# Optimization experiments

Measured on AMD Instinct MI355X. Metric: run time of the kernel, lower is better.

## Reference

```python
import jax, jax.numpy as jnp
import numpy as np

N_PROP, N_GRID, N_KEY, C_FEAT = 128, 216, 4096, 128
RADII = (0.8, 1.6)
NSAMPLES = (16, 16)
C_OUT = 64  # per-branch MLP output channels


def setup_inputs() -> dict:
    key = jax.random.key(0)
    ks = jax.random.split(key, 20)
    s = 0.05
    return {
        "wlh": jax.random.uniform(ks[0], (N_PROP, 3)) * 4.0 + 0.5,
        "center": jax.random.normal(ks[1], (N_PROP, 3)) * 5.0,
        "yaw": jax.random.uniform(ks[2], (N_PROP,)) * 2.0 * np.pi,
        "u": jax.random.uniform(ks[3], (N_PROP, N_GRID, 3)),
        "keypoints_xyz": jax.random.normal(ks[4], (1, N_KEY, 3)) * 5.0,
        "keypoints_features": jax.random.normal(ks[5], (1, C_FEAT, N_KEY)),
        "pn0_w1": jax.random.normal(ks[6], (C_OUT, C_FEAT + 3)) * s,
        "pn0_g1": jnp.ones((C_OUT,)), "pn0_b1": jnp.zeros((C_OUT,)),
        "pn0_w2": jax.random.normal(ks[7], (C_OUT, C_OUT)) * s,
        "pn0_g2": jnp.ones((C_OUT,)), "pn0_b2": jnp.zeros((C_OUT,)),
        "pn1_w1": jax.random.normal(ks[8], (C_OUT, C_FEAT + 3)) * s,
        "pn1_g1": jnp.ones((C_OUT,)), "pn1_b1": jnp.zeros((C_OUT,)),
        "pn1_w2": jax.random.normal(ks[9], (C_OUT, C_OUT)) * s,
        "pn1_g2": jnp.ones((C_OUT,)), "pn1_b2": jnp.zeros((C_OUT,)),
        "red_w1": jax.random.normal(ks[10], (256, N_GRID * 2 * C_OUT)) * 0.01,
        "red_b1": jnp.zeros((256,)),
        "red_w2": jax.random.normal(ks[11], (256, 256)) * s,
        "red_b2": jnp.zeros((256,)),
    }


def reference(wlh, center, yaw, u, keypoints_xyz, keypoints_features,
              pn0_w1, pn0_g1, pn0_b1, pn0_w2, pn0_g2, pn0_b2,
              pn1_w1, pn1_g1, pn1_b1, pn1_w2, pn1_g2, pn1_b2,
              red_w1, red_b1, red_w2, red_b2):
    n, m, _ = u.shape
    # --- sample gridpoints inside proposals and rotate by yaw around z ---
    gp = u * wlh[:, None, :]                                 # (n, m, 3)
    c, s = jnp.cos(yaw), jnp.sin(yaw)
    R = jnp.stack([c, -s, s, c], axis=-1).reshape(-1, 2, 2)   # (n, 2, 2)
    xy = jnp.einsum('njk,nmk->nmj', R, gp[..., :2])
    grid = jnp.concatenate([xy, gp[..., 2:]], -1) + center[:, None, :]
    grid = grid.reshape(-1, 3)                               # (G, 3), G = n*m

    kp = keypoints_xyz[0]                                    # (K, 3)
    kf = jnp.transpose(keypoints_features[0])                # (K, C)
    K = kp.shape[0]

    # squared distances (G, K) without materializing (G, K, 3)
    d2 = (jnp.sum(grid * grid, -1)[:, None]
          + jnp.sum(kp * kp, -1)[None, :]
          - 2.0 * grid @ kp.T)

    def ball_query(radius, nsample):
        # first `nsample` in-radius indices in original order; pad with first
        # hit; all-zeros if no point in radius (pointnet2 CUDA semantics).
        mask = d2 < radius * radius
        cand = jnp.where(mask, jnp.arange(K, dtype=jnp.int32), K)
        srt = jnp.sort(cand, axis=-1)[:, :nsample]           # (G, ns)
        first = srt[:, :1]
        return jnp.where(srt < K, srt, jnp.where(first < K, first, 0))

    def branch(radius, nsample, w1, g1, b1, w2, g2, b2):
        idx = ball_query(radius, nsample)                    # (G, ns)
        xyz = kp[idx] - grid[:, None, :]                     # (G, ns, 3)
        x = jnp.concatenate([xyz, kf[idx]], -1)              # (G, ns, 3+C)
        h = jax.nn.relu(jnp.einsum('gnc,oc->gno', x, w1) * g1 + b1)
        h = jax.nn.relu(jnp.einsum('gnc,oc->gno', h, w2) * g2 + b2)
        return jnp.max(h, axis=1)                            # (G, C_OUT)

    f0 = branch(RADII[0], NSAMPLES[0], pn0_w1, pn0_g1, pn0_b1, pn0_w2, pn0_g2, pn0_b2)
    f1 = branch(RADII[1], NSAMPLES[1], pn1_w1, pn1_g1, pn1_b1, pn1_w2, pn1_g2, pn1_b2)
    pooled = jnp.concatenate([f0, f1], -1)                   # (G, 2*C_OUT)
    Cp = pooled.shape[-1]

    # faithful replication of (1,C,n,m).permute(0,3,1,2).view(1,n,-1)
    t = pooled.reshape(n, m, Cp)                             # gridpoint order (n, m)
    red_in = jnp.transpose(t, (1, 2, 0)).reshape(1, n, m * Cp)

    h = jax.nn.relu(red_in @ red_w1.T + red_b1)
    return jax.nn.relu(h @ red_w2.T + red_b2)                # (1, n, 256)
```

## Files before the change

kernel.cpp:

```cpp
#include <hip/hip_runtime.h>
#include <hip/hip_bf16.h>

typedef unsigned short u16;
typedef unsigned int   u32;
typedef unsigned long long u64;

#define N_PROPC 128
#define N_GRIDC 216
#define G_TOT   27648
#define N_KEYC  4096
#define C_FEATC 128
#define R0SQ    0.64f
#define R1SQ    2.56f
#define BF16_ONES_DWORD 0x3F803F80u

typedef __attribute__((ext_vector_type(8))) short bf16x8;
typedef __attribute__((ext_vector_type(4))) float f32x4;

#if __has_builtin(__builtin_amdgcn_fcmpf)
#define BALLOT_LT(a, b) __builtin_amdgcn_fcmpf((a), (b), 4)
#else
#define BALLOT_LT(a, b) __ballot((a) < (b))
#endif

__device__ __forceinline__ float bf2f(u16 u) {
    return __uint_as_float(((u32)u) << 16);
}
__device__ __forceinline__ u16 f2bf(float f) {
    u32 u = __float_as_uint(f);
    u32 r = (u + 0x7fffu + ((u >> 16) & 1u)) >> 16;
    return (u16)r;
}
__device__ __forceinline__ bool is_bf16(const u32* flagp) {
    return *flagp == BF16_ONES_DWORD;
}
__device__ __forceinline__ float ld(const void* p, int i, bool bf) {
    return bf ? bf2f(((const u16*)p)[i]) : ((const float*)p)[i];
}
__device__ __forceinline__ u16 ldb(const void* p, int i, bool bf) {
    return bf ? ((const u16*)p)[i] : f2bf(((const float*)p)[i]);
}

__global__ __launch_bounds__(256) void prep_fused_kernel(
    const u32* __restrict__ flagp,
    const void* __restrict__ kxyz,
    const void* __restrict__ wlh, const void* __restrict__ center,
    const void* __restrict__ yaw, const void* __restrict__ uu,
    const void* __restrict__ kf,
    const void* __restrict__ w10, const void* __restrict__ g10, const void* __restrict__ b10,
    const void* __restrict__ w20, const void* __restrict__ g20, const void* __restrict__ b20,
    const void* __restrict__ w11, const void* __restrict__ g11, const void* __restrict__ b11,
    const void* __restrict__ w21, const void* __restrict__ g21, const void* __restrict__ b21,
    const void* __restrict__ rw2,
    float4* __restrict__ kp4, float4* __restrict__ grid4, u16* __restrict__ kfT,
    u16* __restrict__ w1mf, u16* __restrict__ w2mf,
    float* __restrict__ g1f, float* __restrict__ b1f,
    float* __restrict__ g2f, float* __restrict__ b2f,
    float* __restrict__ w2rT)
{
    const bool bf = is_bf16(flagp);
    const int bid = blockIdx.x, tid = threadIdx.x;

    if (bid < 16) {
        int k = bid * 256 + tid;
        float x = ld(kxyz, k*3, bf), y = ld(kxyz, k*3+1, bf), z = ld(kxyz, k*3+2, bf);
        kp4[k] = make_float4(x, y, z, 0.0f);
    } else if (bid < 124) {
        int g = (bid - 16) * 256 + tid;
        int n = g / N_GRIDC;
        float ux = ld(uu, g*3, bf), uy = ld(uu, g*3+1, bf), uz = ld(uu, g*3+2, bf);
        float gpx = ux * ld(wlh, n*3, bf);
        float gpy = uy * ld(wlh, n*3+1, bf);
        float gpz = uz * ld(wlh, n*3+2, bf);
        float yv = ld(yaw, n, bf);
        float c = cosf(yv), sn = sinf(yv);
        float x = (c*gpx - sn*gpy) + ld(center, n*3, bf);
        float y = (sn*gpx + c*gpy) + ld(center, n*3+1, bf);
        float z = gpz + ld(center, n*3+2, bf);
        grid4[g] = make_float4(x, y, z, 0.0f);
    } else if (bid < 2172) {
        int t = (bid - 124) * 256 + tid;
        int key = t >> 7, feat = t & 127;
        kfT[t] = ldb(kf, feat * N_KEYC + key, bf);
    } else if (bid < 2174) {
        const int b = bid - 2172;
        const void* w1 = b ? w11 : w10; const void* g1v = b ? g11 : g10;
        const void* w2 = b ? w21 : w20; const void* g2v = b ? g21 : g20;
        const void* b1v = b ? b11 : b10; const void* b2v = b ? b21 : b20;
        for (int f = tid; f < 10240; f += 256) {
            int j = f & 7, t1 = f >> 3;
            int n = t1 & 15, t2 = t1 >> 4;
            int quad = t2 & 3, t3 = t2 >> 2;
            int kt = t3 % 5, nt = t3 / 5;
            int k = kt*32 + quad*8 + j;
            int o = nt*16 + n;
            u16 v = 0;
            if (k < 128)      v = ldb(w1, o*131 + 3 + k, bf);
            else if (k < 131) v = ldb(w1, o*131 + (k - 128), bf);
            w1mf[b*10240 + f] = v;
        }
        for (int f = tid; f < 4096; f += 256) {
            int j = f & 7, t1 = f >> 3;
            int n = t1 & 15, t2 = t1 >> 4;
            int quad = t2 & 3, t3 = t2 >> 2;
            int kt = t3 & 1, nt = t3 >> 1;
            int k = kt*32 + quad*8 + j;
            int o = nt*16 + n;
            w2mf[b*4096 + f] = ldb(w2, o*64 + k, bf);
        }
        if (tid < 64) {
            g1f[b*64 + tid] = ld(g1v, tid, bf);
            b1f[b*64 + tid] = ld(b1v, tid, bf);
            g2f[b*64 + tid] = ld(g2v, tid, bf);
            b2f[b*64 + tid] = ld(b2v, tid, bf);
        }
    } else {
        int t = (bid - 2174) * 256 + tid;
        int o = t & 255, c = t >> 8;
        w2rT[c*256 + o] = ld(rw2, o*256 + c, bf);
    }
}

__global__ __launch_bounds__(256) void ballquery_kernel(
    const float4* __restrict__ kp4,
    const float4* __restrict__ grid4, u16* __restrict__ idx01)
{
    __shared__ __attribute__((aligned(16))) float4 sk[2048];
    const int tid = threadIdx.x;
    const int lane = tid & 63;
    const int wid = tid >> 6;
    const int g0 = blockIdx.x * 16 + wid * 4;
    const float4 gra = grid4[g0];
    const float4 grb = grid4[g0 + 1];
    const float4 grc = grid4[g0 + 2];
    const float4 grd = grid4[g0 + 3];

    u64 m0[4] = {0, 0, 0, 0};
    u64 m1[4] = {0, 0, 0, 0};
    #pragma unroll 1
    for (int pass = 0; pass < 2; ++pass) {
        if (pass) __syncthreads();
        for (int t = tid; t < 2048; t += 256) sk[t] = kp4[pass*2048 + t];
        __syncthreads();
        #pragma unroll
        for (int it = 0; it < 32; ++it) {
            const float4 kv = sk[it*64 + lane];
            const int chunk = pass*32 + it;
            float dx, dy, dz, d;
            dx = kv.x - gra.x; dy = kv.y - gra.y; dz = kv.z - gra.z;
            d = fmaf(dx, dx, fmaf(dy, dy, dz * dz));
            const u64 a1 = BALLOT_LT(d, R1SQ); const u64 a0 = BALLOT_LT(d, R0SQ);
            dx = kv.x - grb.x; dy = kv.y - grb.y; dz = kv.z - grb.z;
            d = fmaf(dx, dx, fmaf(dy, dy, dz * dz));
            const u64 b1m = BALLOT_LT(d, R1SQ); const u64 b0m = BALLOT_LT(d, R0SQ);
            dx = kv.x - grc.x; dy = kv.y - grc.y; dz = kv.z - grc.z;
            d = fmaf(dx, dx, fmaf(dy, dy, dz * dz));
            const u64 c1m = BALLOT_LT(d, R1SQ); const u64 c0m = BALLOT_LT(d, R0SQ);
            dx = kv.x - grd.x; dy = kv.y - grd.y; dz = kv.z - grd.z;
            d = fmaf(dx, dx, fmaf(dy, dy, dz * dz));
            const u64 d1m = BALLOT_LT(d, R1SQ); const u64 d0m = BALLOT_LT(d, R0SQ);
            if (lane == chunk) {
                m1[0] = a1; m0[0] = a0;
                m1[1] = b1m; m0[1] = b0m;
                m1[2] = c1m; m0[2] = c0m;
                m1[3] = d1m; m0[3] = d0m;
            }
        }
    }

    #pragma unroll
    for (int gg = 0; gg < 4; ++gg) {
        const int g = g0 + gg;
        u16* o0 = idx01 + (size_t)g * 16;
        u16* o1 = idx01 + (size_t)G_TOT * 16 + (size_t)g * 16;
        #pragma unroll
        for (int rad = 0; rad < 2; ++rad) {
            u64 mask = rad ? m1[gg] : m0[gg];
            u16* op = rad ? o1 : o0;
            const int cnt = __popcll(mask);
            int inc = cnt;
            #pragma unroll
            for (int d = 1; d < 64; d <<= 1) {
                int t = __shfl_up(inc, d);
                if (lane >= d) inc += t;
            }
            const int pre = inc - cnt;
            int firstk = (cnt > 0 && pre == 0) ? (lane*64 + __ffsll(mask) - 1) : 0x7FFFFFFF;
            #pragma unroll
            for (int d = 32; d >= 1; d >>= 1)
                firstk = min(firstk, __shfl_xor(firstk, d));
            const int total = __shfl(inc, 63);
            u64 mrem = mask;
            int p = pre;
            while (mrem != 0 && p < 16) {
                int j = __ffsll(mrem) - 1;
                op[p] = (u16)(lane*64 + j);
                mrem &= mrem - 1;
                ++p;
            }
            if (lane < 16 && lane >= total)
                op[lane] = (u16)(firstk == 0x7FFFFFFF ? 0 : firstk);
        }
    }
}

__global__ __launch_bounds__(256) void pointnet_mfma_kernel(
    const float4* __restrict__ grid4, const float4* __restrict__ kp4,
    const u16* __restrict__ kfT,
    const u16* __restrict__ w1mf, const u16* __restrict__ w2mf,
    const float* __restrict__ g1f, const float* __restrict__ b1f,
    const float* __restrict__ g2f, const float* __restrict__ b2f,
    const u16* __restrict__ idx01, u16* __restrict__ ATb)
{
    __shared__ __attribute__((aligned(16))) u16 w1s[10240];
    __shared__ __attribute__((aligned(16))) u16 w2s[4096];
    __shared__ __attribute__((aligned(16))) u16 h1s[4][32*72];
    const int tid = threadIdx.x;
    const int branch = blockIdx.y;

    {
        const uint4* s1 = (const uint4*)(w1mf + branch*10240);
        uint4* d1 = (uint4*)w1s;
        for (int t = tid; t < 1280; t += 256) d1[t] = s1[t];
        const uint4* s2 = (const uint4*)(w2mf + branch*4096);
        uint4* d2 = (uint4*)w2s;
        for (int t = tid; t < 512; t += 256) d2[t] = s2[t];
    }
    __syncthreads();

    const int wid = tid >> 6, lane = tid & 63;
    const int n = lane & 15, quad = lane >> 4;
    const int mi = blockIdx.x % N_GRIDC;
    const int nig = blockIdx.x / N_GRIDC;
    const int ni0 = nig*16 + wid*4;

    float g1v[4], b1v[4], g2v[4], b2v[4];
    #pragma unroll
    for (int nt = 0; nt < 4; ++nt) {
        g1v[nt] = g1f[branch*64 + nt*16 + n];
        b1v[nt] = b1f[branch*64 + nt*16 + n];
        g2v[nt] = g2f[branch*64 + nt*16 + n];
        b2v[nt] = b2f[branch*64 + nt*16 + n];
    }

    int idxv[4];
    #pragma unroll
    for (int gg = 0; gg < 4; ++gg) {
        const int g = (ni0 + gg) * N_GRIDC + mi;
        idxv[gg] = idx01[(size_t)branch*(G_TOT*16) + g*16 + n] & (N_KEYC - 1);
    }

    u16* __restrict__ h1w = &h1s[wid][0];

    #pragma unroll 1
    for (int p = 0; p < 2; ++p) {
        const int niA = ni0 + 2*p, niB = niA + 1;
        const int idxA = idxv[2*p], idxB = idxv[2*p + 1];
        const float4 kpA = kp4[idxA];
        const float4 kpB = kp4[idxB];
        const float4 grA = grid4[niA * N_GRIDC + mi];
        const float4 grB = grid4[niB * N_GRIDC + mi];

        const u16* __restrict__ arowA = kfT + idxA * C_FEATC;
        const u16* __restrict__ arowB = kfT + idxB * C_FEATC;
        uint4 arA[4], arB[4];
        #pragma unroll
        for (int kt = 0; kt < 4; ++kt) {
            arA[kt] = *(const uint4*)(arowA + kt*32 + quad*8);
            arB[kt] = *(const uint4*)(arowB + kt*32 + quad*8);
        }

        bf16x8 axyzA = (bf16x8)(short)0, axyzB = (bf16x8)(short)0;
        if (quad == 0) {
            axyzA[0] = (short)f2bf(kpA.x - grA.x);
            axyzA[1] = (short)f2bf(kpA.y - grA.y);
            axyzA[2] = (short)f2bf(kpA.z - grA.z);
            axyzB[0] = (short)f2bf(kpB.x - grB.x);
            axyzB[1] = (short)f2bf(kpB.y - grB.y);
            axyzB[2] = (short)f2bf(kpB.z - grB.z);
        }

        f32x4 accA[4], accB[4];
        #pragma unroll
        for (int nt = 0; nt < 4; ++nt) {
            accA[nt] = (f32x4){0.f, 0.f, 0.f, 0.f};
            accB[nt] = (f32x4){0.f, 0.f, 0.f, 0.f};
        }

        #pragma unroll
        for (int kt = 0; kt < 4; ++kt) {
            bf16x8 aA, aB;
            __builtin_memcpy(&aA, &arA[kt], 16);
            __builtin_memcpy(&aB, &arB[kt], 16);
            #pragma unroll
            for (int nt = 0; nt < 4; ++nt) {
                bf16x8 b = *(const bf16x8*)&w1s[(((nt*5 + kt)*4 + quad)*16 + n)*8];
                accA[nt] = __builtin_amdgcn_mfma_f32_16x16x32_bf16(aA, b, accA[nt], 0, 0, 0);
                accB[nt] = __builtin_amdgcn_mfma_f32_16x16x32_bf16(aB, b, accB[nt], 0, 0, 0);
            }
        }
        #pragma unroll
        for (int nt = 0; nt < 4; ++nt) {
            bf16x8 b = *(const bf16x8*)&w1s[(((nt*5 + 4)*4 + quad)*16 + n)*8];
            accA[nt] = __builtin_amdgcn_mfma_f32_16x16x32_bf16(axyzA, b, accA[nt], 0, 0, 0);
            accB[nt] = __builtin_amdgcn_mfma_f32_16x16x32_bf16(axyzB, b, accB[nt], 0, 0, 0);
        }

        #pragma unroll
        for (int nt = 0; nt < 4; ++nt) {
            #pragma unroll
            for (int r = 0; r < 4; ++r) {
                float vA = fmaxf(fmaf(accA[nt][r], g1v[nt], b1v[nt]), 0.0f);
                float vB = fmaxf(fmaf(accB[nt][r], g1v[nt], b1v[nt]), 0.0f);
                h1w[(quad*4 + r)*72 + nt*16 + n] = f2bf(vA);
                h1w[(16 + quad*4 + r)*72 + nt*16 + n] = f2bf(vB);
            }
        }

        f32x4 cA[4], cB[4];
        #pragma unroll
        for (int nt = 0; nt < 4; ++nt) {
            cA[nt] = (f32x4){0.f, 0.f, 0.f, 0.f};
            cB[nt] = (f32x4){0.f, 0.f, 0.f, 0.f};
        }
        #pragma unroll
        for (int kt = 0; kt < 2; ++kt) {
            bf16x8 a2A = *(const bf16x8*)&h1w[n*72 + kt*32 + quad*8];
            bf16x8 a2B = *(const bf16x8*)&h1w[(16 + n)*72 + kt*32 + quad*8];
            #pragma unroll
            for (int nt = 0; nt < 4; ++nt) {
                bf16x8 b = *(const bf16x8*)&w2s[(((nt*2 + kt)*4 + quad)*16 + n)*8];
                cA[nt] = __builtin_amdgcn_mfma_f32_16x16x32_bf16(a2A, b, cA[nt], 0, 0, 0);
                cB[nt] = __builtin_amdgcn_mfma_f32_16x16x32_bf16(a2B, b, cB[nt], 0, 0, 0);
            }
        }

        #pragma unroll
        for (int nt = 0; nt < 4; ++nt) {
            float vA = fmaxf(fmaxf(fmaxf(fmaf(cA[nt][0], g2v[nt], b2v[nt]), 0.0f),
                                   fmaxf(fmaf(cA[nt][1], g2v[nt], b2v[nt]), 0.0f)),
                             fmaxf(fmaxf(fmaf(cA[nt][2], g2v[nt], b2v[nt]), 0.0f),
                                   fmaxf(fmaf(cA[nt][3], g2v[nt], b2v[nt]), 0.0f)));
            float vB = fmaxf(fmaxf(fmaxf(fmaf(cB[nt][0], g2v[nt], b2v[nt]), 0.0f),
                                   fmaxf(fmaf(cB[nt][1], g2v[nt], b2v[nt]), 0.0f)),
                             fmaxf(fmaxf(fmaf(cB[nt][2], g2v[nt], b2v[nt]), 0.0f),
                                   fmaxf(fmaf(cB[nt][3], g2v[nt], b2v[nt]), 0.0f)));
            vA = fmaxf(vA, __shfl_xor(vA, 16));
            vA = fmaxf(vA, __shfl_xor(vA, 32));
            vB = fmaxf(vB, __shfl_xor(vB, 16));
            vB = fmaxf(vB, __shfl_xor(vB, 32));
            if (lane < 16) {
                const int ci = branch*64 + nt*16 + n;
                ATb[mi*16384 + ci*128 + niA] = f2bf(vA);
                ATb[mi*16384 + ci*128 + niB] = f2bf(vB);
            }
        }
    }
}

__global__ __launch_bounds__(256) void red1_mfma_kernel(
    const u32* __restrict__ flagp,
    const u16* __restrict__ ATb, const void* __restrict__ rw1,
    float* __restrict__ part)
{
    const bool bf = is_bf16(flagp);
    const int tid = threadIdx.x;
    const int wid = tid >> 6, lane = tid & 63;
    const int b = blockIdx.x;
    const int kc = b & 15;
    const int nt = (b >> 4) & 15;
    const int mt = (b >> 8) * 4 + wid;
    const int n = lane & 15, quad = lane >> 4;
    const int o = nt*16 + n;

    const u16* __restrict__ arow = ATb + (size_t)(mt*16 + n) * 27648;

    f32x4 acc = {0.f, 0.f, 0.f, 0.f};
    if (bf) {
        const u16* __restrict__ brow = (const u16*)rw1 + (size_t)o * 27648;
        #pragma unroll 2
        for (int s = 0; s < 54; ++s) {
            const int kk = kc*54 + s;
            uint4 araw = *(const uint4*)(arow + kk*32 + quad*8);
            bf16x8 a;
            __builtin_memcpy(&a, &araw, 16);
            uint4 braw = *(const uint4*)(brow + kk*32 + quad*8);
            bf16x8 bb;
            __builtin_memcpy(&bb, &braw, 16);
            acc = __builtin_amdgcn_mfma_f32_16x16x32_bf16(a, bb, acc, 0, 0, 0);
        }
    } else {
        const float* __restrict__ brow = (const float*)rw1 + (size_t)o * 27648;
        #pragma unroll 2
        for (int s = 0; s < 54; ++s) {
            const int kk = kc*54 + s;
            uint4 araw = *(const uint4*)(arow + kk*32 + quad*8);
            bf16x8 a;
            __builtin_memcpy(&a, &araw, 16);
            const float4 f0 = *(const float4*)(brow + kk*32 + quad*8);
            const float4 f1 = *(const float4*)(brow + kk*32 + quad*8 + 4);
            bf16x8 bb;
            bb[0] = (short)f2bf(f0.x); bb[1] = (short)f2bf(f0.y);
            bb[2] = (short)f2bf(f0.z); bb[3] = (short)f2bf(f0.w);
            bb[4] = (short)f2bf(f1.x); bb[5] = (short)f2bf(f1.y);
            bb[6] = (short)f2bf(f1.z); bb[7] = (short)f2bf(f1.w);
            acc = __builtin_amdgcn_mfma_f32_16x16x32_bf16(a, bb, acc, 0, 0, 0);
        }
    }
    #pragma unroll
    for (int r = 0; r < 4; ++r) {
        const int i = mt*16 + quad*4 + r;
        part[kc*32768 + i*256 + nt*16 + n] = acc[r];
    }
}

__global__ __launch_bounds__(256) void tail_kernel(
    const u32* __restrict__ flagp,
    const float* __restrict__ part, const void* __restrict__ rb1,
    const float* __restrict__ w2rT, const void* __restrict__ rb2,
    void* __restrict__ outp)
{
    __shared__ float hs[256];
    const bool bf = is_bf16(flagp);
    const int o = threadIdx.x, i = blockIdx.x;
    float s = ld(rb1, o, bf);
    #pragma unroll
    for (int kc = 0; kc < 16; ++kc) s += part[kc*32768 + i*256 + o];
    hs[o] = fmaxf(s, 0.0f);
    __syncthreads();
    float s2 = ld(rb2, o, bf);
    #pragma unroll 8
    for (int c = 0; c < 256; ++c)
        s2 = fmaf(hs[c], w2rT[c*256 + o], s2);
    float v = fmaxf(s2, 0.0f);
    if (bf) ((u16*)outp)[i*256 + o] = f2bf(v);
    else    ((float*)outp)[i*256 + o] = v;
}


extern "C" void kernel_launch(void* const* d_in, const int* in_sizes, int n_in,
                              void* d_out, int out_size, void* d_ws, size_t ws_size,
                              hipStream_t stream) {
    const void* wlh    = d_in[0];
    const void* center = d_in[1];
    const void* yaw    = d_in[2];
    const void* uu     = d_in[3];
    const void* kxyz   = d_in[4];
    const void* kfeat  = d_in[5];
    const void* p0w1 = d_in[6];  const void* p0g1 = d_in[7];
    const void* p0b1 = d_in[8];  const void* p0w2 = d_in[9];
    const void* p0g2 = d_in[10]; const void* p0b2 = d_in[11];
    const void* p1w1 = d_in[12]; const void* p1g1 = d_in[13];
    const void* p1b1 = d_in[14]; const void* p1w2 = d_in[15];
    const void* p1g2 = d_in[16]; const void* p1b2 = d_in[17];
    const void* rw1 = d_in[18];
    const void* rb1 = d_in[19];
    const void* rw2 = d_in[20];
    const void* rb2 = d_in[21];
    const u32* flagp = (const u32*)d_in[7];

    char* w = (char*)d_ws;
    float4* kp4   = (float4*)(w + 65536);
    float4* grid4 = (float4*)(w + 131072);
    u16*    kfT   = (u16*)(w + 573440);
    u16*    w1mf  = (u16*)(w + 1622016);
    u16*    w2mf  = (u16*)(w + 1662976);
    float*  g1f   = (float*)(w + 1679360);
    float*  b1f   = (float*)(w + 1679872);
    float*  g2f   = (float*)(w + 1680384);
    float*  b2f   = (float*)(w + 1680896);
    float*  w2rT  = (float*)(w + 1721856);
    u16*    idx01 = (u16*)(w + 1984000);
    u16*    ATb   = (u16*)(w + 3754496);
    float*  part  = (float*)(w + 32066048);

    prep_fused_kernel<<<2430, 256, 0, stream>>>(flagp,
        kxyz, wlh, center, yaw, uu, kfeat,
        p0w1, p0g1, p0b1, p0w2, p0g2, p0b2,
        p1w1, p1g1, p1b1, p1w2, p1g2, p1b2,
        rw2,
        kp4, grid4, kfT,
        w1mf, w2mf, g1f, b1f, g2f, b2f, w2rT);

    ballquery_kernel<<<G_TOT/16, 256, 0, stream>>>(kp4, grid4, idx01);

    dim3 pngrid(G_TOT/16, 2);
    pointnet_mfma_kernel<<<pngrid, 256, 0, stream>>>(grid4, kp4, kfT, w1mf, w2mf,
                                                     g1f, b1f, g2f, b2f, idx01, ATb);

    red1_mfma_kernel<<<512, 256, 0, stream>>>(flagp, ATb, rw1, part);
    tail_kernel<<<128, 256, 0, stream>>>(flagp, part, rb1, w2rT, rb2, d_out);
}
```

Measured before the change: 275.3 us.

## Tile kfT transpose through LDS and keep W2 in registers in pointnet

The key-feature transpose in the prep kernel now stages 64-key tiles through shared memory, so both global reads and writes are coalesced, and the prep grid shrinks accordingly. In the pointnet kernel the W2 weights now live in registers instead of shared memory, and the feature-row loads are moved into the MFMA loop rather than prefetched. A launch-bounds occupancy hint of 4 blocks per CU is added. Together these cut LDS use and register pressure to raise occupancy, at the cost of more VGPRs for W2 and less load latency hiding.

```diff
diff --git a/kernel.cpp b/kernel.cpp
--- a/kernel.cpp
+++ b/kernel.cpp
@@ -58,6 +58,7 @@
     float* __restrict__ g2f, float* __restrict__ b2f,
     float* __restrict__ w2rT)
 {
+    __shared__ u16 tile[64][130];
     const bool bf = is_bf16(flagp);
     const int bid = blockIdx.x, tid = threadIdx.x;
 
@@ -78,12 +79,25 @@
         float y = (sn*gpx + c*gpy) + ld(center, n*3+1, bf);
         float z = gpz + ld(center, n*3+2, bf);
         grid4[g] = make_float4(x, y, z, 0.0f);
-    } else if (bid < 2172) {
-        int t = (bid - 124) * 256 + tid;
-        int key = t >> 7, feat = t & 127;
-        kfT[t] = ldb(kf, feat * N_KEYC + key, bf);
-    } else if (bid < 2174) {
-        const int b = bid - 2172;
+    } else if (bid < 188) {
+        const int key0 = (bid - 124) * 64;
+        #pragma unroll 4
+        for (int rep = 0; rep < 32; ++rep) {
+            int t = rep*256 + tid;
+            int feat = t >> 6;
+            int klo = t & 63;
+            tile[klo][feat] = ldb(kf, feat * N_KEYC + key0 + klo, bf);
+        }
+        __syncthreads();
+        #pragma unroll 4
+        for (int rep = 0; rep < 32; ++rep) {
+            int t = rep*256 + tid;
+            int klo = t >> 7;
+            int feat = t & 127;
+            kfT[(key0 + klo)*128 + feat] = tile[klo][feat];
+        }
+    } else if (bid < 190) {
+        const int b = bid - 188;
         const void* w1 = b ? w11 : w10; const void* g1v = b ? g11 : g10;
         const void* w2 = b ? w21 : w20; const void* g2v = b ? g21 : g20;
         const void* b1v = b ? b11 : b10; const void* b2v = b ? b21 : b20;
@@ -115,7 +129,7 @@
             b2f[b*64 + tid] = ld(b2v, tid, bf);
         }
     } else {
-        int t = (bid - 2174) * 256 + tid;
+        int t = (bid - 190) * 256 + tid;
         int o = t & 255, c = t >> 8;
         w2rT[c*256 + o] = ld(rw2, o*256 + c, bf);
     }
@@ -204,7 +218,7 @@
     }
 }
 
-__global__ __launch_bounds__(256) void pointnet_mfma_kernel(
+__global__ __launch_bounds__(256, 4) void pointnet_mfma_kernel(
     const float4* __restrict__ grid4, const float4* __restrict__ kp4,
     const u16* __restrict__ kfT,
     const u16* __restrict__ w1mf, const u16* __restrict__ w2mf,
@@ -213,7 +227,6 @@
     const u16* __restrict__ idx01, u16* __restrict__ ATb)
 {
     __shared__ __attribute__((aligned(16))) u16 w1s[10240];
-    __shared__ __attribute__((aligned(16))) u16 w2s[4096];
     __shared__ __attribute__((aligned(16))) u16 h1s[4][32*72];
     const int tid = threadIdx.x;
     const int branch = blockIdx.y;
@@ -222,9 +235,6 @@
         const uint4* s1 = (const uint4*)(w1mf + branch*10240);
         uint4* d1 = (uint4*)w1s;
         for (int t = tid; t < 1280; t += 256) d1[t] = s1[t];
-        const uint4* s2 = (const uint4*)(w2mf + branch*4096);
-        uint4* d2 = (uint4*)w2s;
-        for (int t = tid; t < 512; t += 256) d2[t] = s2[t];
     }
     __syncthreads();
 
@@ -233,6 +243,14 @@
     const int mi = blockIdx.x % N_GRIDC;
     const int nig = blockIdx.x / N_GRIDC;
     const int ni0 = nig*16 + wid*4;
+
+    bf16x8 w2r[8];
+    #pragma unroll
+    for (int nt = 0; nt < 4; ++nt)
+        #pragma unroll
+        for (int kt = 0; kt < 2; ++kt)
+            w2r[nt*2 + kt] = *(const bf16x8*)&w2mf[branch*4096 +
+                                (((nt*2 + kt)*4 + quad)*16 + n)*8];
 
     float g1v[4], b1v[4], g2v[4], b2v[4];
     #pragma unroll
@@ -261,15 +279,6 @@
         const float4 grA = grid4[niA * N_GRIDC + mi];
         const float4 grB = grid4[niB * N_GRIDC + mi];
 
-        const u16* __restrict__ arowA = kfT + idxA * C_FEATC;
-        const u16* __restrict__ arowB = kfT + idxB * C_FEATC;
-        uint4 arA[4], arB[4];
-        #pragma unroll
-        for (int kt = 0; kt < 4; ++kt) {
-            arA[kt] = *(const uint4*)(arowA + kt*32 + quad*8);
-            arB[kt] = *(const uint4*)(arowB + kt*32 + quad*8);
-        }
-
         bf16x8 axyzA = (bf16x8)(short)0, axyzB = (bf16x8)(short)0;
         if (quad == 0) {
             axyzA[0] = (short)f2bf(kpA.x - grA.x);
@@ -287,11 +296,15 @@
             accB[nt] = (f32x4){0.f, 0.f, 0.f, 0.f};
         }
 
+        const u16* __restrict__ arowA = kfT + idxA * C_FEATC;
+        const u16* __restrict__ arowB = kfT + idxB * C_FEATC;
         #pragma unroll
         for (int kt = 0; kt < 4; ++kt) {
+            uint4 rA = *(const uint4*)(arowA + kt*32 + quad*8);
+            uint4 rB = *(const uint4*)(arowB + kt*32 + quad*8);
             bf16x8 aA, aB;
-            __builtin_memcpy(&aA, &arA[kt], 16);
-            __builtin_memcpy(&aB, &arB[kt], 16);
+            __builtin_memcpy(&aA, &rA, 16);
+            __builtin_memcpy(&aB, &rB, 16);
             #pragma unroll
             for (int nt = 0; nt < 4; ++nt) {
                 bf16x8 b = *(const bf16x8*)&w1s[(((nt*5 + kt)*4 + quad)*16 + n)*8];
@@ -329,9 +342,8 @@
             bf16x8 a2B = *(const bf16x8*)&h1w[(16 + n)*72 + kt*32 + quad*8];
             #pragma unroll
             for (int nt = 0; nt < 4; ++nt) {
-                bf16x8 b = *(const bf16x8*)&w2s[(((nt*2 + kt)*4 + quad)*16 + n)*8];
-                cA[nt] = __builtin_amdgcn_mfma_f32_16x16x32_bf16(a2A, b, cA[nt], 0, 0, 0);
-                cB[nt] = __builtin_amdgcn_mfma_f32_16x16x32_bf16(a2B, b, cB[nt], 0, 0, 0);
+                cA[nt] = __builtin_amdgcn_mfma_f32_16x16x32_bf16(a2A, w2r[nt*2 + kt], cA[nt], 0, 0, 0);
+                cB[nt] = __builtin_amdgcn_mfma_f32_16x16x32_bf16(a2B, w2r[nt*2 + kt], cB[nt], 0, 0, 0);
             }
         }
 
@@ -474,7 +486,7 @@
     u16*    ATb   = (u16*)(w + 3754496);
     float*  part  = (float*)(w + 32066048);
 
-    prep_fused_kernel<<<2430, 256, 0, stream>>>(flagp,
+    prep_fused_kernel<<<446, 256, 0, stream>>>(flagp,
         kxyz, wlh, center, yaw, uu, kfeat,
         p0w1, p0g1, p0b1, p0w2, p0g2, p0b2,
         p1w1, p1g1, p1b1, p1w2, p1g2, p1b2,
```

Result: slower. 368.4 us (+33.8%).
